# Kernel tuning notes

Measured on AMD Instinct MI355X. Metric: run time of the kernel, lower is better.

Reference implementation:

```python
import jax, jax.numpy as jnp
import numpy as np

H = 16          # num heads
DH = 64         # head dim
D = H * DH      # hidden = 1024


def setup_inputs() -> dict:
    key = jax.random.key(0)
    ks = jax.random.split(key, 9)
    s = 1.0 / np.sqrt(D)
    return {
        "hidden_states": jax.random.normal(ks[0], (4, 2048, D), dtype=jnp.float32),
        "Wq": jax.random.normal(ks[1], (D, D), dtype=jnp.float32) * s,
        "bq": jax.random.normal(ks[2], (D,), dtype=jnp.float32) * 0.02,
        "Wk": jax.random.normal(ks[3], (D, D), dtype=jnp.float32) * s,
        "bk": jax.random.normal(ks[4], (D,), dtype=jnp.float32) * 0.02,
        "Wv": jax.random.normal(ks[5], (D, D), dtype=jnp.float32) * s,
        "bv": jax.random.normal(ks[6], (D,), dtype=jnp.float32) * 0.02,
        "Wo": jax.random.normal(ks[7], (D, D), dtype=jnp.float32) * s,
        "bo": jax.random.normal(ks[8], (D,), dtype=jnp.float32) * 0.02,
    }


def _split_heads(x):  # [B,S,D] -> [B,H,S,DH]
    B, S, _ = x.shape
    return x.reshape(B, S, H, DH).transpose(0, 2, 1, 3)


def reference(hidden_states, Wq, bq, Wk, bk, Wv, bv, Wo, bo):
    # torch Linear: y = x @ W.T + b  (W stored as [out, in])
    q = _split_heads(jnp.einsum('bsd,ed->bse', hidden_states, Wq) + bq)
    k = _split_heads(jnp.einsum('bsd,ed->bse', hidden_states, Wk) + bk)
    v = _split_heads(jnp.einsum('bsd,ed->bse', hidden_states, Wv) + bv)
    scores = jnp.einsum('bhqd,bhkd->bhqk', q, k) / np.sqrt(DH)
    probs = jax.nn.softmax(scores, axis=-1)  # fused softmax+matmul in original
    ctx = jnp.einsum('bhqk,bhkd->bhqd', probs, v)
    B, _, S, _ = ctx.shape
    ctx = ctx.transpose(0, 2, 1, 3).reshape(B, S, D)
    out = jnp.einsum('bsd,ed->bse', ctx, Wo) + bo
    return out  # weights are None (vis=False); dropout rate asserted 0
```

## Files before the change

kernel.cpp:

```cpp
#include <hip/hip_runtime.h>


typedef __bf16 bf16;
typedef __bf16 bf16x8 __attribute__((ext_vector_type(8)));
typedef __bf16 bf16x4 __attribute__((ext_vector_type(4)));
typedef short  short4v __attribute__((ext_vector_type(4)));
typedef float  floatx4 __attribute__((ext_vector_type(4)));

#define NB   4
#define SEQ  2048
#define NH   16
#define DH   64
#define DIM  1024
#define MTOT (NB * SEQ)

#define CEXP 0.18033688f

__device__ __forceinline__ floatx4 zero4() {
    floatx4 z; z[0] = 0.f; z[1] = 0.f; z[2] = 0.f; z[3] = 0.f; return z;
}

__device__ __forceinline__ void load_lds16(const bf16* g, bf16* l) {
    __builtin_amdgcn_global_load_lds(
        (__attribute__((address_space(1))) void*)g,
        (__attribute__((address_space(3))) void*)l,
        16, 0, 0);
}

__device__ __forceinline__ short4v pk4(float a, float b, float c, float d) {
    bf16x4 t; t[0] = (bf16)a; t[1] = (bf16)b; t[2] = (bf16)c; t[3] = (bf16)d;
    return __builtin_bit_cast(short4v, t);
}

__global__ __launch_bounds__(256) void cvt_all(const float* __restrict__ X,
                                               const float* __restrict__ w0,
                                               const float* __restrict__ w1,
                                               const float* __restrict__ w2,
                                               const float* __restrict__ w3,
                                               bf16* __restrict__ Xb,
                                               bf16* __restrict__ Wb) {
    const size_t MD = (size_t)MTOT * DIM;
    const size_t DD = (size_t)DIM * DIM;
    size_t i = ((size_t)blockIdx.x * 256 + threadIdx.x) * 4;
    float4 f; bf16* dst;
    if (i < MD) {
        f = *(const float4*)(X + i);
        dst = Xb + i;
    } else {
        size_t off = i - MD;
        int w = (int)(off >> 20);
        size_t wi = off & (DD - 1);
        const float* ws = (w == 0) ? w0 : (w == 1) ? w1 : (w == 2) ? w2 : w3;
        f = *(const float4*)(ws + wi);
        dst = Wb + off;
    }
    bf16x4 o;
    o[0] = (bf16)f.x; o[1] = (bf16)f.y; o[2] = (bf16)f.z; o[3] = (bf16)f.w;
    *(bf16x4*)dst = o;
}

__global__ __launch_bounds__(256) void gemm_qkv(const bf16* __restrict__ A,
                                                const bf16* __restrict__ W,
                                                const float* __restrict__ bq,
                                                const float* __restrict__ bk,
                                                const float* __restrict__ bv,
                                                bf16* __restrict__ Qo,
                                                bf16* __restrict__ Ko,
                                                bf16* __restrict__ Vt) {
    __shared__ __align__(16) bf16 As[128 * 32];
    __shared__ __align__(16) bf16 Bs[128 * 32];
    __shared__ __align__(16) bf16 Ts[64 * 136];

    const int tid  = threadIdx.x;
    const int wave = tid >> 6, lane = tid & 63;
    const int quad = lane >> 4, l16 = lane & 15;
    const int sel = blockIdx.x >> 3;
    const int nt  = blockIdx.x & 7;
    const int m0 = blockIdx.y * 128, n0 = nt * 128;
    const int wm = (wave & 1) * 64, wn = (wave >> 1) * 64;
    const bf16* Wsel = W + (size_t)(sel * DIM + n0) * DIM;
    const float* bias = (sel == 0) ? bq : (sel == 1) ? bk : bv;
    const float scale = (sel == 0) ? CEXP : 1.0f;

    floatx4 acc[4][4];
#pragma unroll
    for (int mi = 0; mi < 4; mi++)
#pragma unroll
        for (int ni = 0; ni < 4; ni++) acc[mi][ni] = zero4();

    for (int k0 = 0; k0 < DIM; k0 += 32) {
        __syncthreads();
#pragma unroll
        for (int i = 0; i < 2; i++) {
            const int cb = wave * 128 + i * 64;
            const int c  = cb + lane;
            const int row = c >> 2;
            const int kc  = (c & 3) * 8;
            load_lds16(A + (size_t)(m0 + row) * DIM + k0 + kc, &As[cb * 8]);
            load_lds16(Wsel + (size_t)row * DIM + k0 + kc, &Bs[cb * 8]);
        }
        __syncthreads();

        bf16x8 af[4], bfr[4];
#pragma unroll
        for (int mi = 0; mi < 4; mi++)
            af[mi] = *(const bf16x8*)&As[(wm + mi * 16 + l16) * 32 + quad * 8];
#pragma unroll
        for (int ni = 0; ni < 4; ni++)
            bfr[ni] = *(const bf16x8*)&Bs[(wn + ni * 16 + l16) * 32 + quad * 8];
#pragma unroll
        for (int mi = 0; mi < 4; mi++)
#pragma unroll
            for (int ni = 0; ni < 4; ni++)
                acc[mi][ni] = __builtin_amdgcn_mfma_f32_16x16x32_bf16(
                    af[mi], bfr[ni], acc[mi][ni], 0, 0, 0);
    }

    if (sel < 2) {
        bf16* C = (sel == 0) ? Qo : Ko;
#pragma unroll
        for (int mi = 0; mi < 4; mi++) {
            const int rbase = m0 + wm + mi * 16 + quad * 4;
#pragma unroll
            for (int ni = 0; ni < 4; ni++) {
                const int col = n0 + wn + ni * 16 + l16;
                const float bval = bias[col];
#pragma unroll
                for (int i = 0; i < 4; i++)
                    C[(size_t)(rbase + i) * DIM + col] =
                        (bf16)((acc[mi][ni][i] + bval) * scale);
            }
        }
    } else {
        const int b  = blockIdx.y >> 4;
        const int s0 = (blockIdx.y & 15) * 128;
#pragma unroll
        for (int r = 0; r < 2; r++) {
            __syncthreads();
            if ((wave >> 1) == r) {
#pragma unroll
                for (int mi = 0; mi < 4; mi++) {
                    const int m_l = wm + mi * 16 + quad * 4;
#pragma unroll
                    for (int ni = 0; ni < 4; ni++) {
                        const int n_loc = ni * 16 + l16;
                        const float bval = bias[n0 + 64 * r + n_loc];
#pragma unroll
                        for (int i = 0; i < 4; i++)
                            Ts[n_loc * 136 + m_l + i] = (bf16)(acc[mi][ni][i] + bval);
                    }
                }
            }
            __syncthreads();
            const int hh = 2 * nt + r;
            bf16* obase = Vt + ((size_t)(b * NH + hh) * DH) * SEQ + s0;
#pragma unroll
            for (int p = 0; p < 4; p++) {
                const int chunk = p * 256 + tid;
                const int row = chunk >> 4, c0 = (chunk & 15) * 8;
                bf16x8 v = *(const bf16x8*)&Ts[row * 136 + c0];
                *(bf16x8*)(obase + (size_t)row * SEQ + c0) = v;
            }
        }
    }
}

__global__ __launch_bounds__(256) void gemm_out(const bf16* __restrict__ A,
                                                const bf16* __restrict__ W,
                                                const float* __restrict__ bias,
                                                float* __restrict__ C) {
    __shared__ __align__(16) bf16 As[128 * 32];
    __shared__ __align__(16) bf16 Bs[128 * 32];

    const int tid  = threadIdx.x;
    const int wave = tid >> 6, lane = tid & 63;
    const int quad = lane >> 4, l16 = lane & 15;
    const int m0 = blockIdx.y * 128, n0 = blockIdx.x * 128;
    const int wm = (wave & 1) * 64, wn = (wave >> 1) * 64;

    floatx4 acc[4][4];
#pragma unroll
    for (int mi = 0; mi < 4; mi++)
#pragma unroll
        for (int ni = 0; ni < 4; ni++) acc[mi][ni] = zero4();

    for (int k0 = 0; k0 < DIM; k0 += 32) {
        __syncthreads();
#pragma unroll
        for (int i = 0; i < 2; i++) {
            const int cb = wave * 128 + i * 64;
            const int c  = cb + lane;
            const int row = c >> 2;
            const int kc  = (c & 3) * 8;
            load_lds16(A + (size_t)(m0 + row) * DIM + k0 + kc, &As[cb * 8]);
            load_lds16(W + (size_t)(n0 + row) * DIM + k0 + kc, &Bs[cb * 8]);
        }
        __syncthreads();

        bf16x8 af[4], bfr[4];
#pragma unroll
        for (int mi = 0; mi < 4; mi++)
            af[mi] = *(const bf16x8*)&As[(wm + mi * 16 + l16) * 32 + quad * 8];
#pragma unroll
        for (int ni = 0; ni < 4; ni++)
            bfr[ni] = *(const bf16x8*)&Bs[(wn + ni * 16 + l16) * 32 + quad * 8];
#pragma unroll
        for (int mi = 0; mi < 4; mi++)
#pragma unroll
            for (int ni = 0; ni < 4; ni++)
                acc[mi][ni] = __builtin_amdgcn_mfma_f32_16x16x32_bf16(
                    af[mi], bfr[ni], acc[mi][ni], 0, 0, 0);
    }

#pragma unroll
    for (int mi = 0; mi < 4; mi++) {
        const int rbase = m0 + wm + mi * 16 + quad * 4;
#pragma unroll
        for (int ni = 0; ni < 4; ni++) {
            const int col = n0 + wn + ni * 16 + l16;
            const float bval = bias[col];
#pragma unroll
            for (int i = 0; i < 4; i++)
                C[(size_t)(rbase + i) * DIM + col] = acc[mi][ni][i] + bval;
        }
    }
}

__global__ __launch_bounds__(256, 4) void attn_kernel(const bf16* __restrict__ Q,
                                                      const bf16* __restrict__ K,
                                                      const bf16* __restrict__ Vt,
                                                      bf16* __restrict__ Ctx) {
    __shared__ __align__(16) bf16 Ks[2][64 * 64];
    __shared__ __align__(16) bf16 Vs[2][64 * 64];

    const int tid  = threadIdx.x;
    const int wave = tid >> 6, lane = tid & 63;
    const int quad = lane >> 4, l16 = lane & 15;
    const int xcd = blockIdx.x & 7;
    const int j   = blockIdx.x >> 3;
    const int bh  = xcd * 8 + (j >> 4);
    const int qb  = j & 15;
    const int b   = bh >> 4, h = bh & 15;

    const size_t base_bh = (size_t)b * SEQ * DIM + (size_t)h * DH;
    const size_t base_v  = (size_t)bh * DH * SEQ;
    const int qt = qb * 128 + wave * 32;

    bf16x8 aq[2][2];
#pragma unroll
    for (int m = 0; m < 2; m++) {
        const bf16* qp = Q + base_bh + (size_t)(qt + m * 16 + l16) * DIM + quad * 8;
        aq[m][0] = *(const bf16x8*)qp;
        aq[m][1] = *(const bf16x8*)(qp + 32);
    }

    const int sc  = wave * 128 + lane;
    const int sr0 = sc >> 3,        sr1 = (sc + 64) >> 3;
    const int sc0 = (sc & 7) ^ (sr0 & 7), sc1 = ((sc + 64) & 7) ^ (sr1 & 7);
    const bf16* kga = K + base_bh + (size_t)sr0 * DIM + sc0 * 8;
    const bf16* kgb = K + base_bh + (size_t)sr1 * DIM + sc1 * 8;
    const bf16* vga = Vt + base_v + (size_t)sr0 * SEQ + sc0 * 8;
    const bf16* vgb = Vt + base_v + (size_t)sr1 * SEQ + sc1 * 8;
    const int ldsa = (wave * 128) * 8, ldsb = (wave * 128 + 64) * 8;

    int koa[4], kob[4], vo[4][4];
#pragma unroll
    for (int t = 0; t < 4; t++) {
        const int krow = t * 16 + l16;
        koa[t] = (krow * 8 + (quad ^ (krow & 7))) * 8;
        kob[t] = (krow * 8 + ((4 + quad) ^ (krow & 7))) * 8;
#pragma unroll
        for (int dt = 0; dt < 4; dt++) {
            const int d = dt * 16 + l16;
            vo[t][dt] = (d * 8 + ((t * 2 + (quad >> 1)) ^ (d & 7))) * 8
                        + (quad & 1) * 4;
        }
    }

    const short4v ones4 = pk4(1.f, 1.f, 1.f, 1.f);

    floatx4 acc[2][4], accl[2];
#pragma unroll
    for (int m = 0; m < 2; m++) {
        accl[m] = zero4();
#pragma unroll
        for (int dt = 0; dt < 4; dt++) acc[m][dt] = zero4();
    }

    load_lds16(kga, &Ks[0][ldsa]);
    load_lds16(kgb, &Ks[0][ldsb]);
    load_lds16(vga, &Vs[0][ldsa]);
    load_lds16(vgb, &Vs[0][ldsb]);

    for (int it = 0; it < SEQ / 64; it++) {
        __syncthreads();
        const int cur = it & 1;
        if (it + 1 < SEQ / 64) {
            const int nxt = cur ^ 1;
            const size_t kvn = (size_t)(it + 1) * 64;
            load_lds16(kga + kvn * DIM, &Ks[nxt][ldsa]);
            load_lds16(kgb + kvn * DIM, &Ks[nxt][ldsb]);
            load_lds16(vga + kvn, &Vs[nxt][ldsa]);
            load_lds16(vgb + kvn, &Vs[nxt][ldsb]);
        }

#pragma unroll
        for (int t = 0; t < 4; t++) {
            const bf16x8 kb0 = *(const bf16x8*)&Ks[cur][koa[t]];
            const bf16x8 kb1 = *(const bf16x8*)&Ks[cur][kob[t]];
            short4v vb[4];
#pragma unroll
            for (int dt = 0; dt < 4; dt++)
                vb[dt] = __builtin_bit_cast(short4v,
                    *(const bf16x4*)&Vs[cur][vo[t][dt]]);
#pragma unroll
            for (int m = 0; m < 2; m++) {
                floatx4 z = zero4();
                z = __builtin_amdgcn_mfma_f32_16x16x32_bf16(kb0, aq[m][0], z, 0, 0, 0);
                z = __builtin_amdgcn_mfma_f32_16x16x32_bf16(kb1, aq[m][1], z, 0, 0, 0);
                const short4v p = pk4(__builtin_amdgcn_exp2f(z[0]),
                                      __builtin_amdgcn_exp2f(z[1]),
                                      __builtin_amdgcn_exp2f(z[2]),
                                      __builtin_amdgcn_exp2f(z[3]));
#pragma unroll
                for (int dt = 0; dt < 4; dt++)
                    acc[m][dt] = __builtin_amdgcn_mfma_f32_16x16x16bf16_1k(
                        p, vb[dt], acc[m][dt], 0, 0, 0);
                accl[m] = __builtin_amdgcn_mfma_f32_16x16x16bf16_1k(
                    p, ones4, accl[m], 0, 0, 0);
            }
        }
    }

#pragma unroll
    for (int m = 0; m < 2; m++) {
        float inv[4];
#pragma unroll
        for (int i = 0; i < 4; i++) inv[i] = 1.0f / accl[m][i];
        bf16* cp = Ctx + base_bh + (size_t)(qt + m * 16 + quad * 4) * DIM + l16;
#pragma unroll
        for (int i = 0; i < 4; i++)
#pragma unroll
            for (int dt = 0; dt < 4; dt++)
                cp[(size_t)i * DIM + dt * 16] = (bf16)(acc[m][dt][i] * inv[i]);
    }
}

extern "C" void kernel_launch(void* const* d_in, const int* in_sizes, int n_in,
                              void* d_out, int out_size, void* d_ws, size_t ws_size,
                              hipStream_t stream) {
    const float* X  = (const float*)d_in[0];
    const float* Wq = (const float*)d_in[1];
    const float* bq = (const float*)d_in[2];
    const float* Wk = (const float*)d_in[3];
    const float* bk = (const float*)d_in[4];
    const float* Wv = (const float*)d_in[5];
    const float* bv = (const float*)d_in[6];
    const float* Wo = (const float*)d_in[7];
    const float* bo = (const float*)d_in[8];
    float* out = (float*)d_out;

    const size_t MD = (size_t)MTOT * DIM;
    const size_t DD = (size_t)DIM * DIM;

    bf16* Xb  = (bf16*)d_ws;
    bf16* Qb  = Xb + MD;
    bf16* Kb  = Qb + MD;
    bf16* Vtb = Kb + MD;
    bf16* Wqb = Vtb + MD;
    bf16* Wob = Wqb + 3 * DD;
    if (ws_size < (MD * 4 + DD * 4) * sizeof(bf16)) return;

    cvt_all<<<(int)((MD + 4 * DD) / 4 / 256), 256, 0, stream>>>(
        X, Wq, Wk, Wv, Wo, Xb, Wqb);

    gemm_qkv<<<dim3(24, MTOT / 128), 256, 0, stream>>>(Xb, Wqb, bq, bk, bv,
                                                       Qb, Kb, Vtb);

    attn_kernel<<<NB * NH * (SEQ / 128), 256, 0, stream>>>(Qb, Kb, Vtb, Xb);

    gemm_out<<<dim3(8, MTOT / 128), 256, 0, stream>>>(Xb, Wob, bo, out);
}
```

Measured before the change: 294.8 us.

## Use 16x16x32 MFMA for PV product by permuting K row staging

Switches the P·V and row-sum accumulation from 16x16x16 MFMAs to 16x16x32 MFMAs, processing two 16-key groups per step. K rows are permuted during global-to-LDS staging so that the score outputs of two QK MFMAs line up as the k-dimension layout of one wider PV MFMA operand. V fragments become 8-element LDS reads. This halves the PV MFMA instruction count and widens LDS reads, at the cost of more registers held live per step and a subtle index permutation that must match exactly.

```diff
diff --git a/kernel.cpp b/kernel.cpp
--- a/kernel.cpp
+++ b/kernel.cpp
@@ -4,7 +4,6 @@
 typedef __bf16 bf16;
 typedef __bf16 bf16x8 __attribute__((ext_vector_type(8)));
 typedef __bf16 bf16x4 __attribute__((ext_vector_type(4)));
-typedef short  short4v __attribute__((ext_vector_type(4)));
 typedef float  floatx4 __attribute__((ext_vector_type(4)));
 
 #define NB   4
@@ -25,11 +24,6 @@
         (__attribute__((address_space(1))) void*)g,
         (__attribute__((address_space(3))) void*)l,
         16, 0, 0);
-}
-
-__device__ __forceinline__ short4v pk4(float a, float b, float c, float d) {
-    bf16x4 t; t[0] = (bf16)a; t[1] = (bf16)b; t[2] = (bf16)c; t[3] = (bf16)d;
-    return __builtin_bit_cast(short4v, t);
 }
 
 __global__ __launch_bounds__(256) void cvt_all(const float* __restrict__ X,
@@ -254,30 +248,39 @@
         aq[m][1] = *(const bf16x8*)(qp + 32);
     }
 
-    const int sc  = wave * 128 + lane;
-    const int sr0 = sc >> 3,        sr1 = (sc + 64) >> 3;
-    const int sc0 = (sc & 7) ^ (sr0 & 7), sc1 = ((sc + 64) & 7) ^ (sr1 & 7);
-    const bf16* kga = K + base_bh + (size_t)sr0 * DIM + sc0 * 8;
-    const bf16* kgb = K + base_bh + (size_t)sr1 * DIM + sc1 * 8;
-    const bf16* vga = Vt + base_v + (size_t)sr0 * SEQ + sc0 * 8;
-    const bf16* vgb = Vt + base_v + (size_t)sr1 * SEQ + sc1 * 8;
+    const int sc = wave * 128 + lane;
+    int srow[2], scol[2];
+    srow[0] = sc >> 3;        srow[1] = (sc + 64) >> 3;
+    scol[0] = (sc & 7) ^ (srow[0] & 7);
+    scol[1] = ((sc + 64) & 7) ^ (srow[1] & 7);
+    auto kvloc = [](int r) {
+        const int w = r >> 5, rw = r & 31, r4 = rw & 15;
+        return w * 32 + ((rw >> 4) << 2) + ((r4 >> 2) << 3) + (r4 & 3);
+    };
+    const bf16* kga = K + base_bh + (size_t)kvloc(srow[0]) * DIM + scol[0] * 8;
+    const bf16* kgb = K + base_bh + (size_t)kvloc(srow[1]) * DIM + scol[1] * 8;
+    const bf16* vga = Vt + base_v + (size_t)srow[0] * SEQ + scol[0] * 8;
+    const bf16* vgb = Vt + base_v + (size_t)srow[1] * SEQ + scol[1] * 8;
     const int ldsa = (wave * 128) * 8, ldsb = (wave * 128 + 64) * 8;
 
-    int koa[4], kob[4], vo[4][4];
-#pragma unroll
-    for (int t = 0; t < 4; t++) {
-        const int krow = t * 16 + l16;
-        koa[t] = (krow * 8 + (quad ^ (krow & 7))) * 8;
-        kob[t] = (krow * 8 + ((4 + quad) ^ (krow & 7))) * 8;
+    int koa[4], kob[4], vo[2][4];
+#pragma unroll
+    for (int g = 0; g < 4; g++) {
+        const int krow = g * 16 + l16;
+        koa[g] = (krow * 8 + (quad ^ (krow & 7))) * 8;
+        kob[g] = (krow * 8 + ((4 + quad) ^ (krow & 7))) * 8;
+    }
+#pragma unroll
+    for (int w = 0; w < 2; w++)
 #pragma unroll
         for (int dt = 0; dt < 4; dt++) {
             const int d = dt * 16 + l16;
-            vo[t][dt] = (d * 8 + ((t * 2 + (quad >> 1)) ^ (d & 7))) * 8
-                        + (quad & 1) * 4;
-        }
-    }
-
-    const short4v ones4 = pk4(1.f, 1.f, 1.f, 1.f);
+            vo[w][dt] = d * 64 + ((4 * w + quad) ^ (d & 7)) * 8;
+        }
+
+    bf16x8 ones8;
+#pragma unroll
+    for (int i = 0; i < 8; i++) ones8[i] = (bf16)1.0f;
 
     floatx4 acc[2][4], accl[2];
 #pragma unroll
@@ -305,29 +308,39 @@
         }
 
 #pragma unroll
-        for (int t = 0; t < 4; t++) {
-            const bf16x8 kb0 = *(const bf16x8*)&Ks[cur][koa[t]];
-            const bf16x8 kb1 = *(const bf16x8*)&Ks[cur][kob[t]];
-            short4v vb[4];
+        for (int w = 0; w < 2; w++) {
+            const bf16x8 ke0 = *(const bf16x8*)&Ks[cur][koa[2 * w]];
+            const bf16x8 ke1 = *(const bf16x8*)&Ks[cur][kob[2 * w]];
+            const bf16x8 ko0 = *(const bf16x8*)&Ks[cur][koa[2 * w + 1]];
+            const bf16x8 ko1 = *(const bf16x8*)&Ks[cur][kob[2 * w + 1]];
+            bf16x8 pw[2];
+#pragma unroll
+            for (int m = 0; m < 2; m++) {
+                floatx4 sa = zero4(), sb = zero4();
+                sa = __builtin_amdgcn_mfma_f32_16x16x32_bf16(ke0, aq[m][0], sa, 0, 0, 0);
+                sa = __builtin_amdgcn_mfma_f32_16x16x32_bf16(ke1, aq[m][1], sa, 0, 0, 0);
+                sb = __builtin_amdgcn_mfma_f32_16x16x32_bf16(ko0, aq[m][0], sb, 0, 0, 0);
+                sb = __builtin_amdgcn_mfma_f32_16x16x32_bf16(ko1, aq[m][1], sb, 0, 0, 0);
+                bf16x8 p;
+#pragma unroll
+                for (int i = 0; i < 4; i++) {
+                    p[i]     = (bf16)__builtin_amdgcn_exp2f(sa[i]);
+                    p[4 + i] = (bf16)__builtin_amdgcn_exp2f(sb[i]);
+                }
+                pw[m] = p;
+            }
+            bf16x8 vf[4];
 #pragma unroll
             for (int dt = 0; dt < 4; dt++)
-                vb[dt] = __builtin_bit_cast(short4v,
-                    *(const bf16x4*)&Vs[cur][vo[t][dt]]);
+                vf[dt] = *(const bf16x8*)&Vs[cur][vo[w][dt]];
 #pragma unroll
             for (int m = 0; m < 2; m++) {
-                floatx4 z = zero4();
-                z = __builtin_amdgcn_mfma_f32_16x16x32_bf16(kb0, aq[m][0], z, 0, 0, 0);
-                z = __builtin_amdgcn_mfma_f32_16x16x32_bf16(kb1, aq[m][1], z, 0, 0, 0);
-                const short4v p = pk4(__builtin_amdgcn_exp2f(z[0]),
-                                      __builtin_amdgcn_exp2f(z[1]),
-                                      __builtin_amdgcn_exp2f(z[2]),
-                                      __builtin_amdgcn_exp2f(z[3]));
 #pragma unroll
                 for (int dt = 0; dt < 4; dt++)
-                    acc[m][dt] = __builtin_amdgcn_mfma_f32_16x16x16bf16_1k(
-                        p, vb[dt], acc[m][dt], 0, 0, 0);
-                accl[m] = __builtin_amdgcn_mfma_f32_16x16x16bf16_1k(
-                    p, ones4, accl[m], 0, 0, 0);
+                    acc[m][dt] = __builtin_amdgcn_mfma_f32_16x16x32_bf16(
+                        pw[m], vf[dt], acc[m][dt], 0, 0, 0);
+                accl[m] = __builtin_amdgcn_mfma_f32_16x16x32_bf16(
+                    pw[m], ones8, accl[m], 0, 0, 0);
             }
         }
     }
```

After: 270.5 us. 1.09x faster.
